# Performance work log

Hardware: AMD Instinct MI355X
Metric: run time of the kernel (lower is better)

Reference implementation:

```python
import jax, jax.numpy as jnp
import numpy as np

RATIO = 1.0 / 32  # spacial_ratio
HOUT = 7          # pooled_h
WOUT = 7          # pooled_w
S = 2             # sub_bin_size = int(sqrt(n_sampled=4))


def setup_inputs() -> dict:
    key = jax.random.key(0)
    k1, k2, k3, k4, k5, k6 = jax.random.split(key, 6)
    B, C, H, W = 4, 256, 50, 50
    N = 1024
    img_w, img_h = W / RATIO, H / RATIO
    features = jax.random.normal(k1, (B, C, H, W), dtype=jnp.float32)
    b = jax.random.randint(k2, (N,), 0, B).astype(jnp.float32)
    x1 = jax.random.uniform(k3, (N,), minval=0.0, maxval=img_w - 232.0)
    y1 = jax.random.uniform(k4, (N,), minval=0.0, maxval=img_h - 232.0)
    bw = jax.random.uniform(k5, (N,), minval=32.0, maxval=232.0)
    bh = jax.random.uniform(k6, (N,), minval=32.0, maxval=232.0)
    rois = jnp.stack([b, x1, y1, x1 + bw, y1 + bh], axis=1)  # [N, 5]
    return {"features": features, "rois": rois}


def _roi_align(features, rois):
    B, C, H, W = features.shape
    fW = jnp.float32(W)
    fH = jnp.float32(H)
    b_idx = rois[:, 0].astype(jnp.int32)            # [N]
    box = rois[:, 1:] * RATIO                       # [N, 4] in feature coords
    bx1 = jnp.clip(box[:, 0], 0.0, fW)
    by1 = jnp.clip(box[:, 1], 0.0, fH)
    bx2 = jnp.clip(box[:, 2], 0.0, fW)
    by2 = jnp.clip(box[:, 3], 0.0, fH)
    roi_valid = (bx2 - bx1 > 0) & (by2 - by1 > 0)   # [N]
    bin_w = (bx2 - bx1) / WOUT                      # [N]
    bin_h = (by2 - by1) / HOUT

    jj = jnp.arange(WOUT, dtype=jnp.float32)
    ii = jnp.arange(HOUT, dtype=jnp.float32)
    # bin edges; y2/x2 computed from the UNclamped start, then clamped (matches original order)
    x1u = bx1[:, None] + jj * bin_w[:, None]        # [N, WOUT]
    x2b = jnp.clip(x1u + bin_w[:, None], 0.0, fW)
    x1b = jnp.clip(x1u, 0.0, fW)
    y1u = by1[:, None] + ii * bin_h[:, None]        # [N, HOUT]
    y2b = jnp.clip(y1u + bin_h[:, None], 0.0, fH)
    y1b = jnp.clip(y1u, 0.0, fH)
    bin_valid = (y2b > y1b)[:, :, None] & (x2b > x1b)[:, None, :]  # [N, HOUT, WOUT]

    # SxS sample-point centers inside each bin (sub_bin = bin / S, center offset 0.5)
    cc = jnp.arange(S, dtype=jnp.float32) + 0.5
    px = x1b[:, :, None] + cc * (bin_w / S)[:, None, None]  # [N, WOUT, S]
    py = y1b[:, :, None] + cc * (bin_h / S)[:, None, None]  # [N, HOUT, S]

    xl = jnp.clip(jnp.floor(px), 0, W - 1).astype(jnp.int32)
    xh = jnp.clip(xl + 1, 0, W - 1)
    yl = jnp.clip(jnp.floor(py), 0, H - 1).astype(jnp.int32)
    yh = jnp.clip(yl + 1, 0, H - 1)
    wxh = px - xl  # (x - x1)
    wxl = xh - px  # (x2 - x)
    wyb = py - yl  # (y - y1)
    wyt = yh - py  # (y2 - y)

    feats = features.transpose(0, 2, 3, 1)          # [B, H, W, C]
    bI = b_idx[:, None, None, None, None]           # [N,1,1,1,1]
    # x varies over (WOUT, sx) -> broadcast axes (2,4); y over (HOUT, sy) -> axes (1,3)
    XL = xl[:, None, :, None, :]
    XH = xh[:, None, :, None, :]
    YL = yl[:, :, None, :, None]
    YH = yh[:, :, None, :, None]
    WXh = wxh[:, None, :, None, :, None]
    WXl = wxl[:, None, :, None, :, None]
    WYb = wyb[:, :, None, :, None, None]
    WYt = wyt[:, :, None, :, None, None]

    v_tl = feats[bI, YL, XL]   # [N, HOUT, WOUT, S, S, C]
    v_tr = feats[bI, YL, XH]
    v_bl = feats[bI, YH, XL]
    v_br = feats[bI, YH, XH]
    top = WXh * v_tr + WXl * v_tl
    bot = WXh * v_br + WXl * v_bl
    val = WYb * bot + WYt * top                     # [N, HOUT, WOUT, S, S, C]

    pooled = val.max(axis=(3, 4))                   # max over sample grid -> [N, HOUT, WOUT, C]
    mask = bin_valid & roi_valid[:, None, None]
    pooled = jnp.where(mask[..., None], pooled, 0.0)
    return pooled.transpose(0, 3, 1, 2)             # [N, C, HOUT, WOUT]


def reference(features, rois):
    return _roi_align(features, rois)
```

## Files before the change

### kernel.cpp

```cpp
#include <hip/hip_runtime.h>


namespace {

constexpr int B_ = 4, C_ = 256, H_ = 50, W_ = 50;
constexpr int HW = H_ * W_;
constexpr int HO = 7, WO = 7, NBIN = HO * WO;
constexpr int OUT_PER_ROI = C_ * NBIN;
constexpr int LD = 260;
constexpr float RATIO = 1.0f / 32.0f;

__global__ __launch_bounds__(256) void transpose_tiled(
    const float* __restrict__ f, float* __restrict__ ft)
{
    __shared__ float tile[64][65];
    const int bt   = blockIdx.x;
    const int hw_t = bt % 40;
    const int c_t  = (bt / 40) % 4;
    const int b    = bt / 160;
    const int hw0 = hw_t * 64, c0 = c_t * 64;
    const int lx = threadIdx.x & 63;
    const int ly = threadIdx.x >> 6;

#pragma unroll
    for (int k = 0; k < 16; ++k) {
        const int c  = c0 + k * 4 + ly;
        const int hw = hw0 + lx;
        if (hw < HW)
            tile[k * 4 + ly][lx] = f[((size_t)b * C_ + c) * HW + hw];
    }
    __syncthreads();
#pragma unroll
    for (int k = 0; k < 16; ++k) {
        const int hw = hw0 + k * 4 + ly;
        if (hw < HW)
            ft[((size_t)b * HW + hw) * C_ + c0 + lx] = tile[lx][k * 4 + ly];
    }
}

template<int AX, int AY>
__device__ __forceinline__ float4 bin_max(const float4 p[3][3],
                                          const float4 wa, const float4 wb)
{
    float4 s[2][2];
#pragma unroll
    for (int sy = 0; sy < 2; ++sy) {
#pragma unroll
        for (int sx = 0; sx < 2; ++sx) {
            const int xk = AX * sx, yj = AY * sy;
            const float wxh = sx ? wa.y : wa.x;
            const float wxl = sx ? wa.w : wa.z;
            const float wyb = sy ? wb.y : wb.x;
            const float wyt = sy ? wb.w : wb.z;
            const float4 tl = p[yj][xk],     tr = p[yj][xk + 1];
            const float4 bl = p[yj + 1][xk], br = p[yj + 1][xk + 1];
            float4 o;
            o.x = wyb * (wxh * br.x + wxl * bl.x) + wyt * (wxh * tr.x + wxl * tl.x);
            o.y = wyb * (wxh * br.y + wxl * bl.y) + wyt * (wxh * tr.y + wxl * tl.y);
            o.z = wyb * (wxh * br.z + wxl * bl.z) + wyt * (wxh * tr.z + wxl * tl.z);
            o.w = wyb * (wxh * br.w + wxl * bl.w) + wyt * (wxh * tr.w + wxl * tl.w);
            s[sy][sx] = o;
        }
    }
    float4 m;
    m.x = fmaxf(fmaxf(s[0][0].x, s[0][1].x), fmaxf(s[1][0].x, s[1][1].x));
    m.y = fmaxf(fmaxf(s[0][0].y, s[0][1].y), fmaxf(s[1][0].y, s[1][1].y));
    m.z = fmaxf(fmaxf(s[0][0].z, s[0][1].z), fmaxf(s[1][0].z, s[1][1].z));
    m.w = fmaxf(fmaxf(s[0][0].w, s[0][1].w), fmaxf(s[1][0].w, s[1][1].w));
    return m;
}

__global__ __launch_bounds__(256) void roialign_main(
    const float* __restrict__ ft,
    const float* __restrict__ rois,
    float* __restrict__ out)
{
    __shared__ float stage[NBIN * LD];
    __shared__ __align__(16) float    wts[NBIN][8];
    __shared__ __align__(16) unsigned offp[NBIN][12];

    const int n    = blockIdx.x;
    const int tid  = threadIdx.x;
    const int wave = tid >> 6;
    const int lane = tid & 63;
    const float fW = (float)W_, fH = (float)H_;

    if (tid < NBIN) {
        const int ii = tid / WO, jj = tid % WO;
        const float* r = rois + n * 5;
        const float bx1 = fminf(fmaxf(r[1] * RATIO, 0.0f), fW);
        const float by1 = fminf(fmaxf(r[2] * RATIO, 0.0f), fH);
        const float bx2 = fminf(fmaxf(r[3] * RATIO, 0.0f), fW);
        const float by2 = fminf(fmaxf(r[4] * RATIO, 0.0f), fH);
        const bool roi_valid = (bx2 - bx1 > 0.0f) && (by2 - by1 > 0.0f);
        const float bin_w = (bx2 - bx1) * (1.0f / (float)WO);
        const float bin_h = (by2 - by1) * (1.0f / (float)HO);

        const float x1u = bx1 + (float)jj * bin_w;
        const float x1b = fminf(fmaxf(x1u, 0.0f), fW);
        const float x2b = fminf(fmaxf(x1u + bin_w, 0.0f), fW);
        const float y1u = by1 + (float)ii * bin_h;
        const float y1b = fminf(fmaxf(y1u, 0.0f), fH);
        const float y2b = fminf(fmaxf(y1u + bin_h, 0.0f), fH);
        const float vf = (roi_valid && (y2b > y1b) && (x2b > x1b)) ? 1.0f : 0.0f;

        int xl[2], yl[2];
#pragma unroll
        for (int s = 0; s < 2; ++s) {
            const float px = x1b + ((float)s + 0.5f) * (bin_w * 0.5f);
            int l = (int)floorf(px);
            l = min(max(l, 0), W_ - 1);
            const int h = min(l + 1, W_ - 1);
            xl[s] = l;
            wts[tid][0 + s] = vf * (px - (float)l);
            wts[tid][2 + s] = vf * ((float)h - px);

            const float py = y1b + ((float)s + 0.5f) * (bin_h * 0.5f);
            int t = (int)floorf(py);
            t = min(max(t, 0), H_ - 1);
            const int u = min(t + 1, H_ - 1);
            yl[s] = t;
            wts[tid][4 + s] = py - (float)t;
            wts[tid][6 + s] = (float)u - py;
        }
        const int X0 = xl[0], Y0 = yl[0];
        const int ax = min(xl[1] - X0, 1);
        const int ay = min(yl[1] - Y0, 1);
        const int pxs0 = X0, pxs1 = min(X0 + 1, W_ - 1), pxs2 = min(X0 + 2, W_ - 1);
        const int pys0 = Y0, pys1 = min(Y0 + 1, H_ - 1), pys2 = min(Y0 + 2, H_ - 1);
        const int px_[3] = {pxs0, pxs1, pxs2};
        const int py_[3] = {pys0, pys1, pys2};
#pragma unroll
        for (int j = 0; j < 3; ++j)
#pragma unroll
            for (int k = 0; k < 3; ++k)
                offp[tid][j * 3 + k] = (unsigned)(py_[j] * W_ + px_[k]);
        offp[tid][9]  = (unsigned)(ax | (ay << 1));
        offp[tid][10] = 0u;
        offp[tid][11] = 0u;
    }
    __syncthreads();

    int b = (int)rois[n * 5];
    b = min(max(b, 0), B_ - 1);
    const float4* pb = (const float4*)(ft + (size_t)b * HW * C_) + lane;

    for (int bin = wave; bin < NBIN; bin += 4) {
        const float4 wa = *(const float4*)wts[bin];
        const float4 wb = *(const float4*)(wts[bin] + 4);
        const uint4 o0 = *(const uint4*)&offp[bin][0];
        const uint4 o1 = *(const uint4*)&offp[bin][4];
        const uint2 o2 = *(const uint2*)&offp[bin][8];

        float4 p[3][3];
        p[0][0] = pb[(int)o0.x << 6];
        p[0][1] = pb[(int)o0.y << 6];
        p[0][2] = pb[(int)o0.z << 6];
        p[1][0] = pb[(int)o0.w << 6];
        p[1][1] = pb[(int)o1.x << 6];
        p[1][2] = pb[(int)o1.y << 6];
        p[2][0] = pb[(int)o1.z << 6];
        p[2][1] = pb[(int)o1.w << 6];
        p[2][2] = pb[(int)o2.x << 6];

        float4 m;
        switch (o2.y) {
            case 0u:  m = bin_max<0, 0>(p, wa, wb); break;
            case 1u:  m = bin_max<1, 0>(p, wa, wb); break;
            case 2u:  m = bin_max<0, 1>(p, wa, wb); break;
            default:  m = bin_max<1, 1>(p, wa, wb); break;
        }

        *(float4*)&stage[bin * LD + 4 * lane] = m;
    }
    __syncthreads();

    float* outn = out + (size_t)n * OUT_PER_ROI;
    for (int k = tid; k < OUT_PER_ROI; k += 256) {
        const int ch  = k / NBIN;
        const int bin = k - ch * NBIN;
        outn[k] = stage[bin * LD + ch];
    }
}

}

extern "C" void kernel_launch(void* const* d_in, const int* in_sizes, int n_in,
                              void* d_out, int out_size, void* d_ws, size_t ws_size,
                              hipStream_t stream)
{
    const float* feats = (const float*)d_in[0];
    const float* rois  = (const float*)d_in[1];
    float* out = (float*)d_out;
    const int N = in_sizes[1] / 5;
    float* ft = (float*)d_ws;

    hipLaunchKernelGGL(transpose_tiled, dim3(B_ * 4 * 40), dim3(256), 0, stream,
                       feats, ft);
    hipLaunchKernelGGL(roialign_main, dim3(N), dim3(256), 0, stream,
                       ft, rois, out);
}
```

Before: 103.4 us.

## Split each ROI's bins across two blocks and double-issue patch loads

The main kernel now launches two blocks per ROI, each handling 25 or 24 of the 49 bins. This halves the shared staging buffer and raises block count, so more blocks can be resident per CU (launch bounds also request 4 blocks). Each wave now loads the 3x3 patches for two bins before computing either, which gives more memory-level parallelism. The cost is higher register pressure, ROI setup repeated in both blocks, and output writes that are now strided segments instead of one contiguous block.

```diff
diff --git a/kernel.cpp b/kernel.cpp
--- a/kernel.cpp
+++ b/kernel.cpp
@@ -7,6 +7,7 @@
 constexpr int HW = H_ * W_;
 constexpr int HO = 7, WO = 7, NBIN = HO * WO;
 constexpr int OUT_PER_ROI = C_ * NBIN;
+constexpr int MAXB = 25;
 constexpr int LD = 260;
 constexpr float RATIO = 1.0f / 32.0f;
 
@@ -39,7 +40,7 @@
 }
 
 template<int AX, int AY>
-__device__ __forceinline__ float4 bin_max(const float4 p[3][3],
+__device__ __forceinline__ float4 bin_max(const float4 P[9],
                                           const float4 wa, const float4 wb)
 {
     float4 s[2][2];
@@ -52,8 +53,8 @@
             const float wxl = sx ? wa.w : wa.z;
             const float wyb = sy ? wb.y : wb.x;
             const float wyt = sy ? wb.w : wb.z;
-            const float4 tl = p[yj][xk],     tr = p[yj][xk + 1];
-            const float4 bl = p[yj + 1][xk], br = p[yj + 1][xk + 1];
+            const float4 tl = P[yj * 3 + xk],       tr = P[yj * 3 + xk + 1];
+            const float4 bl = P[(yj + 1) * 3 + xk], br = P[(yj + 1) * 3 + xk + 1];
             float4 o;
             o.x = wyb * (wxh * br.x + wxl * bl.x) + wyt * (wxh * tr.x + wxl * tl.x);
             o.y = wyb * (wxh * br.y + wxl * bl.y) + wyt * (wxh * tr.y + wxl * tl.y);
@@ -70,23 +71,38 @@
     return m;
 }
 
-__global__ __launch_bounds__(256) void roialign_main(
+__device__ __forceinline__ float4 bin_max_sel(unsigned fl, const float4 P[9],
+                                              const float4 wa, const float4 wb)
+{
+    switch (fl) {
+        case 0u:  return bin_max<0, 0>(P, wa, wb);
+        case 1u:  return bin_max<1, 0>(P, wa, wb);
+        case 2u:  return bin_max<0, 1>(P, wa, wb);
+        default:  return bin_max<1, 1>(P, wa, wb);
+    }
+}
+
+__global__ __launch_bounds__(256, 4) void roialign_main(
     const float* __restrict__ ft,
     const float* __restrict__ rois,
     float* __restrict__ out)
 {
-    __shared__ float stage[NBIN * LD];
-    __shared__ __align__(16) float    wts[NBIN][8];
-    __shared__ __align__(16) unsigned offp[NBIN][12];
+    __shared__ float stage[MAXB * LD];
+    __shared__ __align__(16) float    wts[MAXB][8];
+    __shared__ __align__(16) unsigned offp[MAXB][12];
 
     const int n    = blockIdx.x;
+    const int half = blockIdx.y;
+    const int base = half * MAXB;
+    const int count = half ? (NBIN - MAXB) : MAXB;
     const int tid  = threadIdx.x;
     const int wave = tid >> 6;
     const int lane = tid & 63;
     const float fW = (float)W_, fH = (float)H_;
 
-    if (tid < NBIN) {
-        const int ii = tid / WO, jj = tid % WO;
+    if (tid < count) {
+        const int gbin = base + tid;
+        const int ii = gbin / WO, jj = gbin % WO;
         const float* r = rois + n * 5;
         const float bx1 = fminf(fmaxf(r[1] * RATIO, 0.0f), fW);
         const float by1 = fminf(fmaxf(r[2] * RATIO, 0.0f), fH);
@@ -126,10 +142,8 @@
         const int X0 = xl[0], Y0 = yl[0];
         const int ax = min(xl[1] - X0, 1);
         const int ay = min(yl[1] - Y0, 1);
-        const int pxs0 = X0, pxs1 = min(X0 + 1, W_ - 1), pxs2 = min(X0 + 2, W_ - 1);
-        const int pys0 = Y0, pys1 = min(Y0 + 1, H_ - 1), pys2 = min(Y0 + 2, H_ - 1);
-        const int px_[3] = {pxs0, pxs1, pxs2};
-        const int py_[3] = {pys0, pys1, pys2};
+        const int px_[3] = {X0, min(X0 + 1, W_ - 1), min(X0 + 2, W_ - 1)};
+        const int py_[3] = {Y0, min(Y0 + 1, H_ - 1), min(Y0 + 2, H_ - 1)};
 #pragma unroll
         for (int j = 0; j < 3; ++j)
 #pragma unroll
@@ -145,41 +159,52 @@
     b = min(max(b, 0), B_ - 1);
     const float4* pb = (const float4*)(ft + (size_t)b * HW * C_) + lane;
 
-    for (int bin = wave; bin < NBIN; bin += 4) {
-        const float4 wa = *(const float4*)wts[bin];
-        const float4 wb = *(const float4*)(wts[bin] + 4);
-        const uint4 o0 = *(const uint4*)&offp[bin][0];
-        const uint4 o1 = *(const uint4*)&offp[bin][4];
-        const uint2 o2 = *(const uint2*)&offp[bin][8];
-
-        float4 p[3][3];
-        p[0][0] = pb[(int)o0.x << 6];
-        p[0][1] = pb[(int)o0.y << 6];
-        p[0][2] = pb[(int)o0.z << 6];
-        p[1][0] = pb[(int)o0.w << 6];
-        p[1][1] = pb[(int)o1.x << 6];
-        p[1][2] = pb[(int)o1.y << 6];
-        p[2][0] = pb[(int)o1.z << 6];
-        p[2][1] = pb[(int)o1.w << 6];
-        p[2][2] = pb[(int)o2.x << 6];
-
-        float4 m;
-        switch (o2.y) {
-            case 0u:  m = bin_max<0, 0>(p, wa, wb); break;
-            case 1u:  m = bin_max<1, 0>(p, wa, wb); break;
-            case 2u:  m = bin_max<0, 1>(p, wa, wb); break;
-            default:  m = bin_max<1, 1>(p, wa, wb); break;
-        }
-
-        *(float4*)&stage[bin * LD + 4 * lane] = m;
+    auto issue_patch = [&](int i, float4 P[9]) {
+        const uint4 o0 = *(const uint4*)&offp[i][0];
+        const uint4 o1 = *(const uint4*)&offp[i][4];
+        const unsigned p22 = offp[i][8];
+        P[0] = pb[(int)o0.x << 6];
+        P[1] = pb[(int)o0.y << 6];
+        P[2] = pb[(int)o0.z << 6];
+        P[3] = pb[(int)o0.w << 6];
+        P[4] = pb[(int)o1.x << 6];
+        P[5] = pb[(int)o1.y << 6];
+        P[6] = pb[(int)o1.z << 6];
+        P[7] = pb[(int)o1.w << 6];
+        P[8] = pb[(int)p22 << 6];
+    };
+
+    for (int i = wave; i < count; i += 8) {
+        const int j = i + 4;
+        float4 PA[9], PB[9];
+        issue_patch(i, PA);
+        if (j < count) issue_patch(j, PB);
+        {
+            const float4 wa = *(const float4*)wts[i];
+            const float4 wb = *(const float4*)(wts[i] + 4);
+            const float4 m = bin_max_sel(offp[i][9], PA, wa, wb);
+            *(float4*)&stage[i * LD + 4 * lane] = m;
+        }
+        if (j < count) {
+            const float4 wa = *(const float4*)wts[j];
+            const float4 wb = *(const float4*)(wts[j] + 4);
+            const float4 m = bin_max_sel(offp[j][9], PB, wa, wb);
+            *(float4*)&stage[j * LD + 4 * lane] = m;
+        }
     }
     __syncthreads();
 
-    float* outn = out + (size_t)n * OUT_PER_ROI;
-    for (int k = tid; k < OUT_PER_ROI; k += 256) {
-        const int ch  = k / NBIN;
-        const int bin = k - ch * NBIN;
-        outn[k] = stage[bin * LD + ch];
+    float* outn = out + (size_t)n * OUT_PER_ROI + base;
+    if (half == 0) {
+        for (int k = tid; k < C_ * 25; k += 256) {
+            const int ch = k / 25, bi = k - ch * 25;
+            outn[ch * NBIN + bi] = stage[bi * LD + ch];
+        }
+    } else {
+        for (int k = tid; k < C_ * 24; k += 256) {
+            const int ch = k / 24, bi = k - ch * 24;
+            outn[ch * NBIN + bi] = stage[bi * LD + ch];
+        }
     }
 }
 
@@ -197,6 +222,6 @@
 
     hipLaunchKernelGGL(transpose_tiled, dim3(B_ * 4 * 40), dim3(256), 0, stream,
                        feats, ft);
-    hipLaunchKernelGGL(roialign_main, dim3(N), dim3(256), 0, stream,
+    hipLaunchKernelGGL(roialign_main, dim3(N, 2), dim3(256), 0, stream,
                        ft, rois, out);
 }
```

Result: slower. 154.1 us (+49.0%).
